# Optimization experiments

Measured on AMD Instinct MI355X. Metric: run time of the kernel, lower is better.

The kernel has to match this reference:

```python
import jax, jax.numpy as jnp
import numpy as np


def _log_g(x):
    # log of g(x) = x + 0.5 for x >= 0, sigmoid(x) for x < 0
    return jnp.where(x >= 0, jnp.log(jax.nn.relu(x) + 0.5), -jax.nn.softplus(-x))


def setup_inputs() -> dict:
    key = jax.random.key(0)
    k1, k2 = jax.random.split(key)
    B, S, D = 4, 4096, 1024
    x = jax.random.normal(k1, (B, S, D), dtype=jnp.float32)
    # torch Linear(dim, 2*dim, bias=False) weight layout: [out, in]
    W = jax.random.normal(k2, (2 * D, D), dtype=jnp.float32) * (1.0 / np.sqrt(D))
    return {"x": x, "W": W}


def reference(x, W):
    # x: [B, S, D], W: [2D, D]
    hg = jnp.einsum('bsd,ed->bse', x, W)            # [B, S, 2D]
    hidden, gate = jnp.split(hg, 2, axis=-1)        # each [B, S, D]

    log_coeffs = -jax.nn.softplus(gate)             # log(1 - sigmoid(gate))
    log_z = -jax.nn.softplus(-gate)                 # log(sigmoid(gate))
    log_values = log_z + _log_g(hidden)

    # Heinsen associative scan in log space over the sequence axis
    a_star = jnp.cumsum(log_coeffs, axis=1)
    log_h = a_star + jax.lax.cumlogsumexp(log_values - a_star, axis=1)
    out = jnp.exp(log_h)                            # [B, S, D]; to_out is Identity
    return out
```

## Files before the change

kernel.cpp:

```cpp
#include <hip/hip_runtime.h>
#include <hip/hip_bf16.h>
#include <hip/hip_fp16.h>
#include <cstdint>

typedef unsigned short us;
typedef us   us8 __attribute__((ext_vector_type(8)));
typedef short s8v __attribute__((ext_vector_type(8)));
typedef float f4v __attribute__((ext_vector_type(4)));
typedef __fp16 pk2 __attribute__((ext_vector_type(2)));

#define BB 4
#define SS 4096
#define DD 1024
#define MM (BB * SS)
#define NN (2 * DD)
#define KK DD

#define BM 128
#define BN 128
#define BK 64

#define CHUNK 32
#define NC (SS / CHUNK)
#define DP (DD / 2)
#define BDP (BB * DP)

__device__ inline us f2bf(float f) {
  unsigned u = __float_as_uint(f);
  u += 0x7fffu + ((u >> 16) & 1u);
  return (us)(u >> 16);
}

__global__ __launch_bounds__(256) void cvt_both(const float* __restrict__ x,
                                                const float* __restrict__ W,
                                                us* __restrict__ xb,
                                                us* __restrict__ wb,
                                                long nx) {
  long i = ((long)blockIdx.x * 256 + threadIdx.x) * 8;
  const float* in;
  us* out;
  if (i < nx) { in = x + i; out = xb + i; }
  else        { in = W + (i - nx); out = wb + (i - nx); }
  const float4* p = (const float4*)in;
  float4 a = p[0], b = p[1];
  us8 o;
  o[0] = f2bf(a.x); o[1] = f2bf(a.y); o[2] = f2bf(a.z); o[3] = f2bf(a.w);
  o[4] = f2bf(b.x); o[5] = f2bf(b.y); o[6] = f2bf(b.z); o[7] = f2bf(b.w);
  *(us8*)out = o;
}

#define GLD16(g, l)                                                        \
  __builtin_amdgcn_global_load_lds(                                        \
      (const __attribute__((address_space(1))) void*)(g),                  \
      (__attribute__((address_space(3))) void*)(l), 16, 0, 0)

__device__ inline void gate_cv(float hid, float gat, float& coef, float& v) {
  float e = __expf(gat);
  coef = __builtin_amdgcn_rcpf(1.0f + e);
  float z = 1.0f - coef;
  float eh = __expf(hid < 0.0f ? hid : 0.0f);
  float gneg = eh * __builtin_amdgcn_rcpf(1.0f + eh);
  float g = (hid >= 0.0f) ? (hid + 0.5f) : gneg;
  v = z * g;
}

__global__ __launch_bounds__(256) void gemm_fused(const us* __restrict__ A,
                                                  const us* __restrict__ B,
                                                  unsigned* __restrict__ cv) {
  __shared__ __align__(16) us As[BM * BK];
  __shared__ __align__(16) us Bs[BN * BK];

  const int tid  = threadIdx.x;
  const int lane = tid & 63;
  const int w    = tid >> 6;
  const int wm   = w & 1;
  const int wn   = w >> 1;
  const long bm  = (long)blockIdx.x * BM;
  const int  d0  = blockIdx.y * 64;

  const int srow = lane >> 3;
  const int sseg = (lane & 7) ^ srow;

  const int fr = lane & 15;
  const int fq = lane >> 4;

  int aoff[4][2], boff[4][2];
#pragma unroll
  for (int mt = 0; mt < 4; ++mt) {
    int row = wm * 64 + mt * 16 + fr;
#pragma unroll
    for (int kk = 0; kk < 2; ++kk) {
      int seg = kk * 4 + fq;
      aoff[mt][kk] = row * BK + ((seg ^ (row & 7)) * 8);
    }
  }
#pragma unroll
  for (int nt = 0; nt < 4; ++nt) {
    int row = wn * 64 + nt * 16 + fr;
#pragma unroll
    for (int kk = 0; kk < 2; ++kk) {
      int seg = kk * 4 + fq;
      boff[nt][kk] = row * BK + ((seg ^ (row & 7)) * 8);
    }
  }

  f4v acc[4][4] = {};

  const us* Ap[4];
  const us* Bp[4];
#pragma unroll
  for (int i = 0; i < 4; ++i) {
    int lr = w * 32 + i * 8 + srow;
    Ap[i] = A + (bm + lr) * (long)KK + sseg * 8;
    int wrow = d0 + ((lr >> 5) << 4) + (lr & 15) + (((lr >> 4) & 1) << 10);
    Bp[i] = B + (long)wrow * KK + sseg * 8;
  }

  for (int kt = 0; kt < KK / BK; ++kt) {
    const int k0 = kt * BK;
    __syncthreads();
#pragma unroll
    for (int i = 0; i < 4; ++i) {
      GLD16(Ap[i] + k0, &As[(w * 32 + i * 8) * BK]);
      GLD16(Bp[i] + k0, &Bs[(w * 32 + i * 8) * BK]);
    }
    __syncthreads();

#pragma unroll
    for (int kk = 0; kk < 2; ++kk) {
      s8v af[4], bf[4];
#pragma unroll
      for (int mt = 0; mt < 4; ++mt) af[mt] = *(const s8v*)&As[aoff[mt][kk]];
#pragma unroll
      for (int nt = 0; nt < 4; ++nt) bf[nt] = *(const s8v*)&Bs[boff[nt][kk]];
#pragma unroll
      for (int mt = 0; mt < 4; ++mt)
#pragma unroll
        for (int nt = 0; nt < 4; ++nt)
          acc[mt][nt] = __builtin_amdgcn_mfma_f32_16x16x32_bf16(
              af[mt], bf[nt], acc[mt][nt], 0, 0, 0);
    }
  }

#pragma unroll
  for (int mt = 0; mt < 4; ++mt) {
    long rb = bm + wm * 64 + mt * 16 + fq * 4;
#pragma unroll
    for (int p = 0; p < 2; ++p) {
      int d = d0 + (wn * 2 + p) * 16 + fr;
      f4v hv = acc[mt][2 * p];
      f4v gv = acc[mt][2 * p + 1];
#pragma unroll
      for (int r = 0; r < 4; ++r) {
        float coef, v;
        gate_cv(hv[r], gv[r], coef, v);
        pk2 pk = __builtin_amdgcn_cvt_pkrtz(coef, v);
        cv[(rb + r) * (size_t)DD + d] = __builtin_bit_cast(unsigned, pk);
      }
    }
  }
}

__global__ __launch_bounds__(256) void scan_pass1(const uint2* __restrict__ cv,
                                                  float2* __restrict__ cp,
                                                  float2* __restrict__ ch) {
  const int dp = blockIdx.x * 256 + threadIdx.x;
  const int c = blockIdx.y;
  const int b = blockIdx.z;
  const uint2* base = cv + ((size_t)b * SS + (size_t)c * CHUNK) * DP + dp;
  float P0 = 1.0f, h0 = 0.0f, P1 = 1.0f, h1 = 0.0f;
#pragma unroll 8
  for (int t = 0; t < CHUNK; ++t) {
    uint2 u = base[(size_t)t * DP];
    __half2 a = *(__half2*)&u.x;
    __half2 bq = *(__half2*)&u.y;
    float c0 = __half2float(a.x), v0 = __half2float(a.y);
    float c1 = __half2float(bq.x), v1 = __half2float(bq.y);
    h0 = fmaf(c0, h0, v0);  P0 *= c0;
    h1 = fmaf(c1, h1, v1);  P1 *= c1;
  }
  const int idx = c * BDP + b * DP + dp;
  cp[idx] = make_float2(P0, P1);
  ch[idx] = make_float2(h0, h1);
}

__global__ __launch_bounds__(256) void scan_pass2(const float2* __restrict__ cp,
                                                  const float2* __restrict__ ch,
                                                  float2* __restrict__ carry) {
  const int bdp = blockIdx.x * 256 + threadIdx.x;
  float h0 = 0.0f, h1 = 0.0f;
  for (int c = 0; c < NC; ++c) {
    carry[c * BDP + bdp] = make_float2(h0, h1);
    float2 P = cp[c * BDP + bdp];
    float2 H = ch[c * BDP + bdp];
    h0 = fmaf(P.x, h0, H.x);
    h1 = fmaf(P.y, h1, H.y);
  }
}

__global__ __launch_bounds__(256) void scan_pass3(const uint2* __restrict__ cv,
                                                  const float2* __restrict__ carry,
                                                  float2* __restrict__ out) {
  const int dp = blockIdx.x * 256 + threadIdx.x;
  const int c = blockIdx.y;
  const int b = blockIdx.z;
  const uint2* base = cv + ((size_t)b * SS + (size_t)c * CHUNK) * DP + dp;
  float2* obase = out + ((size_t)b * SS + (size_t)c * CHUNK) * DP + dp;
  float2 hc = carry[c * BDP + b * DP + dp];
  float h0 = hc.x, h1 = hc.y;
#pragma unroll 8
  for (int t = 0; t < CHUNK; ++t) {
    uint2 u = base[(size_t)t * DP];
    __half2 a = *(__half2*)&u.x;
    __half2 bq = *(__half2*)&u.y;
    h0 = fmaf(__half2float(a.x), h0, __half2float(a.y));
    h1 = fmaf(__half2float(bq.x), h1, __half2float(bq.y));
    obase[(size_t)t * DP] = make_float2(h0, h1);
  }
}

extern "C" void kernel_launch(void* const* d_in, const int* in_sizes, int n_in,
                              void* d_out, int out_size, void* d_ws, size_t ws_size,
                              hipStream_t stream) {
  const float* x = (const float*)d_in[0];
  const float* W = (const float*)d_in[1];
  float2* out = (float2*)d_out;

  const long nx = (long)MM * KK;
  const long nw = (long)NN * KK;

  char* ws = (char*)d_ws;
  unsigned* cv = (unsigned*)ws;      ws += (size_t)MM * DD * sizeof(unsigned);
  us* xb = (us*)ws;                  ws += (size_t)nx * sizeof(us);
  us* wb = (us*)ws;                  ws += (size_t)nw * sizeof(us);
  float2* cp = (float2*)ws;          ws += (size_t)NC * BDP * sizeof(float2);
  float2* chh = (float2*)ws;         ws += (size_t)NC * BDP * sizeof(float2);
  float2* carry = (float2*)ws;       ws += (size_t)NC * BDP * sizeof(float2);

  cvt_both<<<(int)((nx + nw) / 8 / 256), 256, 0, stream>>>(x, W, xb, wb, nx);

  gemm_fused<<<dim3(MM / BM, DD / 64), 256, 0, stream>>>(xb, wb, cv);

  scan_pass1<<<dim3(DP / 256, NC, BB), 256, 0, stream>>>((const uint2*)cv, cp, chh);
  scan_pass2<<<dim3(BDP / 256), 256, 0, stream>>>(cp, chh, carry);
  scan_pass3<<<dim3(DP / 256, NC, BB), 256, 0, stream>>>((const uint2*)cv, carry, out);
}
```

Before: 255.1 us.

## Fuse scan pass1 chunk reduction into GEMM epilogue via LDS staging

The GEMM epilogue now stages the packed (coef, value) tile in shared memory, writes it to global memory with coalesced 16-byte stores, and computes each 32-row chunk's product and partial state directly from LDS. This removes the separate scan_pass1 kernel and its full re-read of the cv buffer. Chunk summaries change from float2 pairs to a per-column float layout. The cost is extra LDS traffic and synchronisation at the end of the GEMM.

```diff
diff --git a/kernel.cpp b/kernel.cpp
--- a/kernel.cpp
+++ b/kernel.cpp
@@ -22,8 +22,8 @@
 
 #define CHUNK 32
 #define NC (SS / CHUNK)
+#define BDD (BB * DD)
 #define DP (DD / 2)
-#define BDP (BB * DP)
 
 __device__ inline us f2bf(float f) {
   unsigned u = __float_as_uint(f);
@@ -66,9 +66,13 @@
 
 __global__ __launch_bounds__(256) void gemm_fused(const us* __restrict__ A,
                                                   const us* __restrict__ B,
-                                                  unsigned* __restrict__ cv) {
-  __shared__ __align__(16) us As[BM * BK];
-  __shared__ __align__(16) us Bs[BN * BK];
+                                                  unsigned* __restrict__ cv,
+                                                  float* __restrict__ cp,
+                                                  float* __restrict__ ch) {
+  __shared__ __align__(16) us smem[BM * BK + BN * BK];
+  us* As = smem;
+  us* Bs = smem + BM * BK;
+  unsigned* T = (unsigned*)smem;
 
   const int tid  = threadIdx.x;
   const int lane = tid & 63;
@@ -117,12 +121,13 @@
   }
 
   for (int kt = 0; kt < KK / BK; ++kt) {
-    const int k0 = kt * BK;
     __syncthreads();
 #pragma unroll
     for (int i = 0; i < 4; ++i) {
-      GLD16(Ap[i] + k0, &As[(w * 32 + i * 8) * BK]);
-      GLD16(Bp[i] + k0, &Bs[(w * 32 + i * 8) * BK]);
+      GLD16(Ap[i], &As[(w * 32 + i * 8) * BK]);
+      GLD16(Bp[i], &Bs[(w * 32 + i * 8) * BK]);
+      Ap[i] += BK;
+      Bp[i] += BK;
     }
     __syncthreads();
 
@@ -142,12 +147,13 @@
     }
   }
 
+  __syncthreads();
 #pragma unroll
   for (int mt = 0; mt < 4; ++mt) {
-    long rb = bm + wm * 64 + mt * 16 + fq * 4;
+    int lr0 = wm * 64 + mt * 16 + fq * 4;
 #pragma unroll
     for (int p = 0; p < 2; ++p) {
-      int d = d0 + (wn * 2 + p) * 16 + fr;
+      int ld = (wn * 2 + p) * 16 + fr;
       f4v hv = acc[mt][2 * p];
       f4v gv = acc[mt][2 * p + 1];
 #pragma unroll
@@ -155,58 +161,61 @@
         float coef, v;
         gate_cv(hv[r], gv[r], coef, v);
         pk2 pk = __builtin_amdgcn_cvt_pkrtz(coef, v);
-        cv[(rb + r) * (size_t)DD + d] = __builtin_bit_cast(unsigned, pk);
+        T[(lr0 + r) * 64 + ld] = __builtin_bit_cast(unsigned, pk);
       }
     }
   }
-}
-
-__global__ __launch_bounds__(256) void scan_pass1(const uint2* __restrict__ cv,
-                                                  float2* __restrict__ cp,
-                                                  float2* __restrict__ ch) {
-  const int dp = blockIdx.x * 256 + threadIdx.x;
-  const int c = blockIdx.y;
-  const int b = blockIdx.z;
-  const uint2* base = cv + ((size_t)b * SS + (size_t)c * CHUNK) * DP + dp;
-  float P0 = 1.0f, h0 = 0.0f, P1 = 1.0f, h1 = 0.0f;
-#pragma unroll 8
-  for (int t = 0; t < CHUNK; ++t) {
-    uint2 u = base[(size_t)t * DP];
-    __half2 a = *(__half2*)&u.x;
-    __half2 bq = *(__half2*)&u.y;
-    float c0 = __half2float(a.x), v0 = __half2float(a.y);
-    float c1 = __half2float(bq.x), v1 = __half2float(bq.y);
-    h0 = fmaf(c0, h0, v0);  P0 *= c0;
-    h1 = fmaf(c1, h1, v1);  P1 *= c1;
-  }
-  const int idx = c * BDP + b * DP + dp;
-  cp[idx] = make_float2(P0, P1);
-  ch[idx] = make_float2(h0, h1);
-}
-
-__global__ __launch_bounds__(256) void scan_pass2(const float2* __restrict__ cp,
-                                                  const float2* __restrict__ ch,
-                                                  float2* __restrict__ carry) {
-  const int bdp = blockIdx.x * 256 + threadIdx.x;
-  float h0 = 0.0f, h1 = 0.0f;
+  __syncthreads();
+
+#pragma unroll
+  for (int j = 0; j < 8; ++j) {
+    int chunk = j * 256 + tid;
+    int row = chunk >> 4;
+    int q   = chunk & 15;
+    uint4 val = *(const uint4*)&T[row * 64 + q * 4];
+    *(uint4*)(cv + (size_t)(bm + row) * DD + d0 + q * 4) = val;
+  }
+
+  {
+    const int d = tid & 63;
+    const int c = tid >> 6;
+    float P = 1.0f, h = 0.0f;
+#pragma unroll
+    for (int i = 0; i < CHUNK; ++i) {
+      unsigned u = T[(c * CHUNK + i) * 64 + d];
+      __half2 hv = *(__half2*)&u;
+      float cf = __half2float(hv.x);
+      h = fmaf(cf, h, __half2float(hv.y));
+      P *= cf;
+    }
+    const int b  = (int)(bm / SS);
+    const int cg = (int)((bm % SS) / CHUNK) + c;
+    const int idx = cg * BDD + b * DD + d0 + d;
+    cp[idx] = P;
+    ch[idx] = h;
+  }
+}
+
+__global__ __launch_bounds__(256) void scan_pass2(const float* __restrict__ cp,
+                                                  const float* __restrict__ ch,
+                                                  float* __restrict__ carry) {
+  const int bd = blockIdx.x * 256 + threadIdx.x;
+  float h = 0.0f;
   for (int c = 0; c < NC; ++c) {
-    carry[c * BDP + bdp] = make_float2(h0, h1);
-    float2 P = cp[c * BDP + bdp];
-    float2 H = ch[c * BDP + bdp];
-    h0 = fmaf(P.x, h0, H.x);
-    h1 = fmaf(P.y, h1, H.y);
+    carry[c * BDD + bd] = h;
+    h = fmaf(cp[c * BDD + bd], h, ch[c * BDD + bd]);
   }
 }
 
 __global__ __launch_bounds__(256) void scan_pass3(const uint2* __restrict__ cv,
-                                                  const float2* __restrict__ carry,
+                                                  const float* __restrict__ carry,
                                                   float2* __restrict__ out) {
   const int dp = blockIdx.x * 256 + threadIdx.x;
   const int c = blockIdx.y;
   const int b = blockIdx.z;
   const uint2* base = cv + ((size_t)b * SS + (size_t)c * CHUNK) * DP + dp;
   float2* obase = out + ((size_t)b * SS + (size_t)c * CHUNK) * DP + dp;
-  float2 hc = carry[c * BDP + b * DP + dp];
+  float2 hc = *(const float2*)&carry[c * BDD + b * DD + 2 * dp];
   float h0 = hc.x, h1 = hc.y;
 #pragma unroll 8
   for (int t = 0; t < CHUNK; ++t) {
@@ -233,15 +242,14 @@
   unsigned* cv = (unsigned*)ws;      ws += (size_t)MM * DD * sizeof(unsigned);
   us* xb = (us*)ws;                  ws += (size_t)nx * sizeof(us);
   us* wb = (us*)ws;                  ws += (size_t)nw * sizeof(us);
-  float2* cp = (float2*)ws;          ws += (size_t)NC * BDP * sizeof(float2);
-  float2* chh = (float2*)ws;         ws += (size_t)NC * BDP * sizeof(float2);
-  float2* carry = (float2*)ws;       ws += (size_t)NC * BDP * sizeof(float2);
+  float* cp = (float*)ws;            ws += (size_t)NC * BDD * sizeof(float);
+  float* chh = (float*)ws;           ws += (size_t)NC * BDD * sizeof(float);
+  float* carry = (float*)ws;         ws += (size_t)NC * BDD * sizeof(float);
 
   cvt_both<<<(int)((nx + nw) / 8 / 256), 256, 0, stream>>>(x, W, xb, wb, nx);
 
-  gemm_fused<<<dim3(MM / BM, DD / 64), 256, 0, stream>>>(xb, wb, cv);
-
-  scan_pass1<<<dim3(DP / 256, NC, BB), 256, 0, stream>>>((const uint2*)cv, cp, chh);
-  scan_pass2<<<dim3(BDP / 256), 256, 0, stream>>>(cp, chh, carry);
+  gemm_fused<<<dim3(MM / BM, DD / 64), 256, 0, stream>>>(xb, wb, cv, cp, chh);
+
+  scan_pass2<<<dim3(BDD / 256), 256, 0, stream>>>(cp, chh, carry);
   scan_pass3<<<dim3(DP / 256, NC, BB), 256, 0, stream>>>((const uint2*)cv, carry, out);
 }
```

Measured after the change: 234.2 us. -8.2%, faster.
